# Kernel optimization log

Hardware: AMD Instinct MI355X
Metric: run time of the kernel (lower is better)

Reference implementation:

```python
import jax, jax.numpy as jnp
import numpy as np

N, S, E, H = 8, 1024, 1024, 16
DK = E // H


def setup_inputs() -> dict:
    key = jax.random.key(0)
    ks = jax.random.split(key, 12)
    scale = 1.0 / np.sqrt(E)
    inp = {
        "q": jax.random.normal(ks[0], (N, S, E), jnp.float32),
        "k": jax.random.normal(ks[1], (N, S, E), jnp.float32),
        "v": jax.random.normal(ks[2], (N, S, E), jnp.float32),
        "attn_mask": jax.random.randint(ks[3], (N, S, S), 0, 2).astype(bool),
        "wq": jax.random.normal(ks[4], (E, E), jnp.float32) * scale,
        "bq": jnp.zeros((E,), jnp.float32),
        "wk": jax.random.normal(ks[5], (E, E), jnp.float32) * scale,
        "bk": jnp.zeros((E,), jnp.float32),
        "wv": jax.random.normal(ks[6], (E, E), jnp.float32) * scale,
        "bv": jnp.zeros((E,), jnp.float32),
        "wo": jax.random.normal(ks[7], (E, E), jnp.float32) * scale,
        "bo": jnp.zeros((E,), jnp.float32),
    }
    return inp


def reference(q, k, v, attn_mask, wq, bq, wk, bk, wv, bv, wo, bo):
    # Linear projections (weights stored as (E_in, E_out)), split into heads.
    qh = (q @ wq + bq).reshape(N, S, H, DK).transpose(0, 2, 1, 3)  # (N,H,S,DK)
    kh = (k @ wk + bk).reshape(N, S, H, DK).transpose(0, 2, 1, 3)
    vh = (v @ wv + bv).reshape(N, S, H, DK).transpose(0, 2, 1, 3)
    logits = jnp.einsum("nhsd,nhtd->nhst", qh, kh) / np.sqrt(DK)  # (N,H,S,S)
    eps = 1e9
    logits = jnp.where(attn_mask[:, None, :, :], -eps, logits)
    attn_weights = jax.nn.softmax(logits, axis=-1)
    # dropout layers are identity in eval mode
    o = jnp.einsum("nhst,nhtd->nhsd", attn_weights, vh)  # (N,H,S,DK)
    o = o.transpose(0, 2, 1, 3).reshape(N, S, E)
    o = o @ wo + bo
    return o, attn_weights
```

## Files before the change

kernel.cpp:

```cpp
#include <hip/hip_runtime.h>
#include <cstdint>
#include <cstddef>

#define NB 8
#define SL 1024
#define ED 1024
#define NH 16
#define DKH 64

typedef __attribute__((ext_vector_type(4))) float f32x4;
typedef __attribute__((ext_vector_type(8))) short short8;

__device__ __forceinline__ unsigned short bf16_rn(float x) {
    unsigned int u = __float_as_uint(x);
    u += 0x7FFFu + ((u >> 16) & 1u);
    return (unsigned short)(u >> 16);
}
__device__ __forceinline__ float bf16_f(unsigned short h) {
    return __uint_as_float(((unsigned int)h) << 16);
}
__device__ __forceinline__ void split2(float x, unsigned short& hi, unsigned short& lo) {
    unsigned short h = bf16_rn(x);
    hi = h;
    lo = bf16_rn(x - bf16_f(h));
}

__device__ __forceinline__ void dma16(const unsigned short* src, unsigned short* dst) {
    __builtin_amdgcn_global_load_lds(
        (const __attribute__((address_space(1))) void*)src,
        (__attribute__((address_space(3))) void*)dst,
        16, 0, 0);
}

template<int ROWS>
__device__ __forceinline__ void dma_plane(
    const unsigned short* __restrict__ g, unsigned short* l,
    int ld, int r0, int k0, int wave, int lane)
{
    for (int i = wave; i < ROWS / 16; i += 4) {
        const unsigned short* src =
            g + (size_t)(r0 + i * 16 + (lane >> 2)) * ld + k0 + (lane & 3) * 8;
        dma16(src, l + i * 512);
    }
}

template<bool APRE, int BM, int BN, int WR, int WC, int ROWG, int COLT>
__device__ __forceinline__ void gemm_core3(
    unsigned short* smem,
    const float* __restrict__ Af,
    const unsigned short* __restrict__ Ahg, const unsigned short* __restrict__ Alg,
    int lda,
    const unsigned short* __restrict__ Bhg, const unsigned short* __restrict__ Blg,
    int ldb, int Kd, int m0, int n0,
    f32x4 (&acc)[ROWG][COLT])
{
    static_assert(WR * WC == 4, "4 waves");
    static_assert(16 * ROWG * WR == BM, "rows");
    static_assert(16 * COLT * WC == BN, "cols");
    static_assert(APRE || BM == 128, "fp32 staging assumes BM=128");

    constexpr int ASZ = BM * 32;
    constexpr int BSZ = BN * 32;
    unsigned short* Ah = smem;
    unsigned short* Al = smem + 2 * ASZ;
    unsigned short* Bh = smem + 4 * ASZ;
    unsigned short* Bl = smem + 4 * ASZ + 2 * BSZ;

    const int tid  = threadIdx.x;
    const int wave = tid >> 6;
    const int lane = tid & 63;
    const int quad = lane >> 4;
    const int l16  = lane & 15;
    const int wr   = wave / WC;
    const int wc   = wave % WC;

#pragma unroll
    for (int g = 0; g < ROWG; g++)
#pragma unroll
        for (int jt = 0; jt < COLT; jt++) acc[g][jt] = (f32x4)(0.0f);

    const int ar  = tid >> 1;
    const int acb = (tid & 1) * 2;

    auto load_a = [&](int kk, float4 st[4]) {
        const float* p = Af + (size_t)(m0 + ar) * lda + kk + (tid & 1) * 16;
        st[0] = *(const float4*)(p + 0);
        st[1] = *(const float4*)(p + 4);
        st[2] = *(const float4*)(p + 8);
        st[3] = *(const float4*)(p + 12);
    };
    auto write_a = [&](int b, const float4 st[4]) {
        unsigned short* dh = Ah + b * ASZ;
        unsigned short* dl = Al + b * ASZ;
#pragma unroll
        for (int w = 0; w < 2; w++) {
            const int csw = (acb + w) ^ ((ar >> 1) & 3);
            const float4 u0 = st[2 * w], u1 = st[2 * w + 1];
            short8 h8, l8;
            unsigned short h, l;
            split2(u0.x, h, l); h8[0] = (short)h; l8[0] = (short)l;
            split2(u0.y, h, l); h8[1] = (short)h; l8[1] = (short)l;
            split2(u0.z, h, l); h8[2] = (short)h; l8[2] = (short)l;
            split2(u0.w, h, l); h8[3] = (short)h; l8[3] = (short)l;
            split2(u1.x, h, l); h8[4] = (short)h; l8[4] = (short)l;
            split2(u1.y, h, l); h8[5] = (short)h; l8[5] = (short)l;
            split2(u1.z, h, l); h8[6] = (short)h; l8[6] = (short)l;
            split2(u1.w, h, l); h8[7] = (short)h; l8[7] = (short)l;
            *(short8*)&dh[ar * 32 + csw * 8] = h8;
            *(short8*)&dl[ar * 32 + csw * 8] = l8;
        }
    };
    auto stage_b = [&](int b, int kk) {
        dma_plane<BN>(Bhg, Bh + b * BSZ, ldb, n0, kk, wave, lane);
        dma_plane<BN>(Blg, Bl + b * BSZ, ldb, n0, kk, wave, lane);
    };
    auto stage_a_dma = [&](int b, int kk) {
        dma_plane<BM>(Ahg, Ah + b * ASZ, lda, m0, kk, wave, lane);
        dma_plane<BM>(Alg, Al + b * ASZ, lda, m0, kk, wave, lane);
    };

    if constexpr (APRE) {
        stage_a_dma(0, 0);
    } else {
        float4 st[4];
        load_a(0, st);
        write_a(0, st);
    }
    stage_b(0, 0);
    __syncthreads();

    int buf = 0;
    for (int k0 = 0; k0 < Kd; k0 += 32) {
        const int nk = k0 + 32;
        float4 st[4];
        if (nk < Kd) {
            if constexpr (APRE) stage_a_dma(buf ^ 1, nk);
            else                load_a(nk, st);
            stage_b(buf ^ 1, nk);
        }
        const unsigned short* pAh = Ah + buf * ASZ;
        const unsigned short* pAl = Al + buf * ASZ;
        const unsigned short* pBh = Bh + buf * BSZ;
        const unsigned short* pBl = Bl + buf * BSZ;
        short8 ah[ROWG], al[ROWG];
#pragma unroll
        for (int g = 0; g < ROWG; g++) {
            const int row = wr * (16 * ROWG) + g * 16 + l16;
            int co;
            if constexpr (APRE) co = quad * 8;
            else                co = (quad ^ ((row >> 1) & 3)) * 8;
            ah[g] = *(const short8*)&pAh[row * 32 + co];
            al[g] = *(const short8*)&pAl[row * 32 + co];
        }
#pragma unroll
        for (int jt = 0; jt < COLT; jt++) {
            const int brow = wc * (16 * COLT) + jt * 16 + l16;
            const short8 bh = *(const short8*)&pBh[brow * 32 + quad * 8];
            const short8 bl = *(const short8*)&pBl[brow * 32 + quad * 8];
#pragma unroll
            for (int g = 0; g < ROWG; g++) {
                acc[g][jt] = __builtin_amdgcn_mfma_f32_16x16x32_bf16(al[g], bh, acc[g][jt], 0, 0, 0);
                acc[g][jt] = __builtin_amdgcn_mfma_f32_16x16x32_bf16(ah[g], bl, acc[g][jt], 0, 0, 0);
                acc[g][jt] = __builtin_amdgcn_mfma_f32_16x16x32_bf16(ah[g], bh, acc[g][jt], 0, 0, 0);
            }
        }
        if constexpr (!APRE) {
            if (nk < Kd) write_a(buf ^ 1, st);
        }
        __syncthreads();
        buf ^= 1;
    }
}

__global__ __launch_bounds__(256)
void k_wsplitT(const float* __restrict__ W,
               unsigned short* __restrict__ Th, unsigned short* __restrict__ Tl)
{
    __shared__ float tile[64 * 65];
    const int n0 = blockIdx.x * 64;
    const int k0 = blockIdx.y * 64;
    const int tid = threadIdx.x;
    for (int i = tid; i < 64 * 64; i += 256) {
        const int rk = i >> 6, cn = i & 63;
        tile[rk * 65 + cn] = W[(size_t)(k0 + rk) * ED + n0 + cn];
    }
    __syncthreads();
    for (int i = tid; i < 64 * 64; i += 256) {
        const int rn = i >> 6, ck = i & 63;
        unsigned short h, l;
        split2(tile[ck * 65 + rn], h, l);
        Th[(size_t)(n0 + rn) * ED + k0 + ck] = h;
        Tl[(size_t)(n0 + rn) * ED + k0 + ck] = l;
    }
}

__global__ __launch_bounds__(256)
void k_projQK(const float* __restrict__ X,
              const unsigned short* __restrict__ Wh, const unsigned short* __restrict__ Wl,
              const float* __restrict__ bias,
              unsigned short* __restrict__ Oh, unsigned short* __restrict__ Ol)
{
    __shared__ unsigned short smem[(128 + 128) * 128];
    const int m0 = blockIdx.x * 128;
    const int n0 = blockIdx.y * 128;
    f32x4 acc[4][4];
    gemm_core3<false, 128, 128, 2, 2, 4, 4>(smem, X, nullptr, nullptr, ED,
                                            Wh, Wl, ED, ED, m0, n0, acc);

    const int tid = threadIdx.x, wave = tid >> 6, lane = tid & 63;
    const int quad = lane >> 4, l16 = lane & 15;
    const int wr = wave >> 1, wc = wave & 1;
#pragma unroll
    for (int jt = 0; jt < 4; jt++) {
        const int col = n0 + wc * 64 + jt * 16 + l16;
        const int h = col >> 6, d = col & 63;
        const float b = bias[col];
#pragma unroll
        for (int g = 0; g < 4; g++) {
#pragma unroll
            for (int rr = 0; rr < 4; rr++) {
                const int m = m0 + wr * 64 + g * 16 + quad * 4 + rr;
                const int n = m >> 10, s = m & 1023;
                const size_t idx = (((size_t)(n * NH + h)) * SL + s) * DKH + d;
                unsigned short hh, ll;
                split2(acc[g][jt][rr] + b, hh, ll);
                Oh[idx] = hh;
                Ol[idx] = ll;
            }
        }
    }
}

__global__ __launch_bounds__(256)
void k_projV(const float* __restrict__ X,
             const unsigned short* __restrict__ Wh, const unsigned short* __restrict__ Wl,
             const float* __restrict__ bias,
             unsigned short* __restrict__ Th, unsigned short* __restrict__ Tl)
{
    __shared__ unsigned short smem[(128 + 64) * 128];
    const int m0 = blockIdx.x * 128;
    const int n0 = blockIdx.y * 64;
    f32x4 acc[2][4];
    gemm_core3<false, 128, 64, 4, 1, 2, 4>(smem, X, nullptr, nullptr, ED,
                                           Wh, Wl, ED, ED, m0, n0, acc);

    unsigned int* T = (unsigned int*)smem;
    const int tid = threadIdx.x, wave = tid >> 6, lane = tid & 63;
    const int quad = lane >> 4, l16 = lane & 15;
#pragma unroll
    for (int jt = 0; jt < 4; jt++) {
        const int d = jt * 16 + l16;
        const float b = bias[n0 + d];
#pragma unroll
        for (int g = 0; g < 2; g++) {
#pragma unroll
            for (int rr = 0; rr < 4; rr++) {
                const int sl = wave * 32 + g * 16 + quad * 4 + rr;
                unsigned short hh, ll;
                split2(acc[g][jt][rr] + b, hh, ll);
                T[sl * 65 + d] = (unsigned int)hh | ((unsigned int)ll << 16);
            }
        }
    }
    __syncthreads();
    const int d  = tid >> 2;
    const int sc = (tid & 3) * 32;
    const int ghead = (m0 >> 10) * NH + (n0 >> 6);
    const size_t rowbase = ((size_t)ghead * DKH + d) * SL + (m0 & 1023) + sc;
#pragma unroll
    for (int c = 0; c < 4; c++) {
        short8 h8, l8;
#pragma unroll
        for (int i = 0; i < 8; i++) {
            const unsigned int u = T[(sc + c * 8 + i) * 65 + d];
            h8[i] = (short)(u & 0xFFFFu);
            l8[i] = (short)(u >> 16);
        }
        *(short8*)(Th + rowbase + c * 8) = h8;
        *(short8*)(Tl + rowbase + c * 8) = l8;
    }
}

__global__ __launch_bounds__(256)
void k_logits(const unsigned short* __restrict__ qh_h, const unsigned short* __restrict__ qh_l,
              const unsigned short* __restrict__ kh_h, const unsigned short* __restrict__ kh_l,
              const int* __restrict__ mask, float* __restrict__ attn)
{
    __shared__ unsigned short smem[(128 + 128) * 128];
    const int head = blockIdx.z;
    const int n = head >> 4;
    const int m0 = blockIdx.x * 128;
    const int n0 = blockIdx.y * 128;
    const size_t hb = (size_t)head * SL * DKH;
    f32x4 acc[4][4];
    gemm_core3<true, 128, 128, 2, 2, 4, 4>(smem, nullptr, qh_h + hb, qh_l + hb, DKH,
                                           kh_h + hb, kh_l + hb, DKH, DKH, m0, n0, acc);

    const int tid = threadIdx.x, wave = tid >> 6, lane = tid & 63;
    const int quad = lane >> 4, l16 = lane & 15;
    const int wr = wave >> 1, wc = wave & 1;
    const float scale = 0.125f;
#pragma unroll
    for (int jt = 0; jt < 4; jt++) {
        const int t = n0 + wc * 64 + jt * 16 + l16;
#pragma unroll
        for (int g = 0; g < 4; g++) {
#pragma unroll
            for (int rr = 0; rr < 4; rr++) {
                const int s = m0 + wr * 64 + g * 16 + quad * 4 + rr;
                float vv = acc[g][jt][rr] * scale;
                if (mask[((size_t)n * SL + s) * SL + t]) vv = -1e9f;
                attn[((size_t)head * SL + s) * SL + t] = vv;
            }
        }
    }
}

__global__ __launch_bounds__(256)
void k_softmax(float* __restrict__ attn)
{
    const int tid = threadIdx.x;
    const int wave = tid >> 6, lane = tid & 63;
    const size_t row = (size_t)blockIdx.x * 4 + wave;
    float* p = attn + row * SL;

    float4 v[4];
    float mx = -3.4e38f;
#pragma unroll
    for (int i = 0; i < 4; i++) {
        v[i] = *(const float4*)(p + lane * 4 + i * 256);
        mx = fmaxf(mx, fmaxf(fmaxf(v[i].x, v[i].y), fmaxf(v[i].z, v[i].w)));
    }
#pragma unroll
    for (int o = 32; o > 0; o >>= 1) mx = fmaxf(mx, __shfl_xor(mx, o));

    float sum = 0.0f;
#pragma unroll
    for (int i = 0; i < 4; i++) {
        v[i].x = __expf(v[i].x - mx);
        v[i].y = __expf(v[i].y - mx);
        v[i].z = __expf(v[i].z - mx);
        v[i].w = __expf(v[i].w - mx);
        sum += v[i].x + v[i].y + v[i].z + v[i].w;
    }
#pragma unroll
    for (int o = 32; o > 0; o >>= 1) sum += __shfl_xor(sum, o);

    const float inv = 1.0f / sum;
#pragma unroll
    for (int i = 0; i < 4; i++) {
        v[i].x *= inv; v[i].y *= inv; v[i].z *= inv; v[i].w *= inv;
        *(float4*)(p + lane * 4 + i * 256) = v[i];
    }
}

__global__ __launch_bounds__(256)
void k_pv(const float* __restrict__ attn,
          const unsigned short* __restrict__ vTh, const unsigned short* __restrict__ vTl,
          unsigned short* __restrict__ Oh, unsigned short* __restrict__ Ol)
{
    __shared__ unsigned short smem[(128 + 64) * 128];
    const int head = blockIdx.z;
    const int m0 = blockIdx.x * 128;
    const float* P = attn + (size_t)head * SL * SL;
    const unsigned short* Bh = vTh + (size_t)head * DKH * SL;
    const unsigned short* Bl = vTl + (size_t)head * DKH * SL;
    f32x4 acc[2][4];
    gemm_core3<false, 128, 64, 4, 1, 2, 4>(smem, P, nullptr, nullptr, SL,
                                           Bh, Bl, SL, SL, m0, 0, acc);

    const int tid = threadIdx.x, wave = tid >> 6, lane = tid & 63;
    const int quad = lane >> 4, l16 = lane & 15;
    const int n = head >> 4, h = head & 15;
#pragma unroll
    for (int jt = 0; jt < 4; jt++) {
        const int d = jt * 16 + l16;
#pragma unroll
        for (int g = 0; g < 2; g++) {
#pragma unroll
            for (int rr = 0; rr < 4; rr++) {
                const int s = m0 + wave * 32 + g * 16 + quad * 4 + rr;
                const size_t idx = ((size_t)n * SL + s) * ED + h * DKH + d;
                unsigned short hh, ll;
                split2(acc[g][jt][rr], hh, ll);
                Oh[idx] = hh;
                Ol[idx] = ll;
            }
        }
    }
}

__global__ __launch_bounds__(256)
void k_outproj(const unsigned short* __restrict__ Ah, const unsigned short* __restrict__ Al,
               const unsigned short* __restrict__ Wh, const unsigned short* __restrict__ Wl,
               const float* __restrict__ bias, float* __restrict__ out)
{
    __shared__ unsigned short smem[(128 + 128) * 128];
    const int m0 = blockIdx.x * 128;
    const int n0 = blockIdx.y * 128;
    f32x4 acc[4][4];
    gemm_core3<true, 128, 128, 2, 2, 4, 4>(smem, nullptr, Ah, Al, ED,
                                           Wh, Wl, ED, ED, m0, n0, acc);

    const int tid = threadIdx.x, wave = tid >> 6, lane = tid & 63;
    const int quad = lane >> 4, l16 = lane & 15;
    const int wr = wave >> 1, wc = wave & 1;
#pragma unroll
    for (int jt = 0; jt < 4; jt++) {
        const int col = n0 + wc * 64 + jt * 16 + l16;
        const float b = bias[col];
#pragma unroll
        for (int g = 0; g < 4; g++) {
#pragma unroll
            for (int rr = 0; rr < 4; rr++) {
                const int m = m0 + wr * 64 + g * 16 + quad * 4 + rr;
                out[(size_t)m * ED + col] = acc[g][jt][rr] + b;
            }
        }
    }
}

extern "C" void kernel_launch(void* const* d_in, const int* in_sizes, int n_in,
                              void* d_out, int out_size, void* d_ws, size_t ws_size,
                              hipStream_t stream) {
    const float* q    = (const float*)d_in[0];
    const float* k    = (const float*)d_in[1];
    const float* v    = (const float*)d_in[2];
    const int*   mask = (const int*)d_in[3];
    const float* wq = (const float*)d_in[4];
    const float* bq = (const float*)d_in[5];
    const float* wk = (const float*)d_in[6];
    const float* bk = (const float*)d_in[7];
    const float* wv = (const float*)d_in[8];
    const float* bv = (const float*)d_in[9];
    const float* wo = (const float*)d_in[10];
    const float* bo = (const float*)d_in[11];

    float* out  = (float*)d_out;
    float* attn = out + (size_t)NB * SL * ED;

    unsigned short* w = (unsigned short*)d_ws;
    const size_t WPL = (size_t)ED * ED;
    unsigned short* wqT_h = w + 0 * WPL;
    unsigned short* wqT_l = w + 1 * WPL;
    unsigned short* wkT_h = w + 2 * WPL;
    unsigned short* wkT_l = w + 3 * WPL;
    unsigned short* wvT_h = w + 4 * WPL;
    unsigned short* wvT_l = w + 5 * WPL;
    unsigned short* woT_h = w + 6 * WPL;
    unsigned short* woT_l = w + 7 * WPL;
    unsigned short* base  = w + 8 * WPL;
    const size_t HPL = (size_t)NB * NH * SL * DKH;
    unsigned short* qh_h = base + 0 * HPL;
    unsigned short* qh_l = base + 1 * HPL;
    unsigned short* kh_h = base + 2 * HPL;
    unsigned short* kh_l = base + 3 * HPL;
    unsigned short* vT_h = base + 4 * HPL;
    unsigned short* vT_l = base + 5 * HPL;
    unsigned short* oh_h = qh_h;
    unsigned short* oh_l = qh_l;

    const dim3 blk(256);
    const dim3 gw(ED / 64, ED / 64);
    hipLaunchKernelGGL(k_wsplitT, gw, blk, 0, stream, wq, wqT_h, wqT_l);
    hipLaunchKernelGGL(k_wsplitT, gw, blk, 0, stream, wk, wkT_h, wkT_l);
    hipLaunchKernelGGL(k_wsplitT, gw, blk, 0, stream, wv, wvT_h, wvT_l);
    hipLaunchKernelGGL(k_wsplitT, gw, blk, 0, stream, wo, woT_h, woT_l);

    const dim3 gproj(8192 / 128, ED / 128);
    hipLaunchKernelGGL(k_projQK, gproj, blk, 0, stream, q, wqT_h, wqT_l, bq, qh_h, qh_l);
    hipLaunchKernelGGL(k_projQK, gproj, blk, 0, stream, k, wkT_h, wkT_l, bk, kh_h, kh_l);

    const dim3 gprojV(8192 / 128, ED / 64);
    hipLaunchKernelGGL(k_projV, gprojV, blk, 0, stream, v, wvT_h, wvT_l, bv, vT_h, vT_l);

    const dim3 glog(SL / 128, SL / 128, NB * NH);
    hipLaunchKernelGGL(k_logits, glog, blk, 0, stream, qh_h, qh_l, kh_h, kh_l, mask, attn);

    hipLaunchKernelGGL(k_softmax, dim3(NB * NH * SL / 4), blk, 0, stream, attn);

    const dim3 gpv(SL / 128, 1, NB * NH);
    hipLaunchKernelGGL(k_pv, gpv, blk, 0, stream, attn, vT_h, vT_l, oh_h, oh_l);

    hipLaunchKernelGGL(k_outproj, gproj, blk, 0, stream, oh_h, oh_l, woT_h, woT_l, bo, out);
}
```

Before: 1.495 ms.

## Fuse logits, masked softmax and PV into one attention kernel

Replaces the separate logits, softmax and PV kernels with one fused kernel. Each 512-thread block handles 32 query rows of one head across the full key length, computes masked logits in registers, does a cross-wave softmax reduction through shared memory, writes the attention weights once, and accumulates P@V from the same registers. This removes the write-read-write-read round trips of the 512MB attention matrix through HBM. The cost is that K and V are read straight from global memory with no LDS staging, each block re-reads them, and register pressure is high.

```diff
diff --git a/kernel.cpp b/kernel.cpp
--- a/kernel.cpp
+++ b/kernel.cpp
@@ -10,6 +10,7 @@
 
 typedef __attribute__((ext_vector_type(4))) float f32x4;
 typedef __attribute__((ext_vector_type(8))) short short8;
+typedef __attribute__((ext_vector_type(4))) short short4v;
 
 __device__ __forceinline__ unsigned short bf16_rn(float x) {
     unsigned int u = __float_as_uint(x);
@@ -281,112 +282,209 @@
     }
 }
 
-__global__ __launch_bounds__(256)
-void k_logits(const unsigned short* __restrict__ qh_h, const unsigned short* __restrict__ qh_l,
-              const unsigned short* __restrict__ kh_h, const unsigned short* __restrict__ kh_l,
-              const int* __restrict__ mask, float* __restrict__ attn)
-{
-    __shared__ unsigned short smem[(128 + 128) * 128];
-    const int head = blockIdx.z;
-    const int n = head >> 4;
-    const int m0 = blockIdx.x * 128;
-    const int n0 = blockIdx.y * 128;
-    const size_t hb = (size_t)head * SL * DKH;
-    f32x4 acc[4][4];
-    gemm_core3<true, 128, 128, 2, 2, 4, 4>(smem, nullptr, qh_h + hb, qh_l + hb, DKH,
-                                           kh_h + hb, kh_l + hb, DKH, DKH, m0, n0, acc);
-
+#define PFW 68
+__global__ __launch_bounds__(512)
+void k_attn_fused(const unsigned short* __restrict__ qh_h, const unsigned short* __restrict__ qh_l,
+                  const unsigned short* __restrict__ kh_h, const unsigned short* __restrict__ kh_l,
+                  const unsigned short* __restrict__ vT_h, const unsigned short* __restrict__ vT_l,
+                  const int* __restrict__ mask, float* __restrict__ attn,
+                  unsigned short* __restrict__ Oh, unsigned short* __restrict__ Ol)
+{
+    __shared__ float Pf[8][16][PFW];
+    __shared__ float MX[4][32];
+    __shared__ float SMm[4][32];
+
+    const int head = blockIdx.y;
+    const int n = head >> 4, h = head & 15;
+    const int m0 = blockIdx.x * 32;
     const int tid = threadIdx.x, wave = tid >> 6, lane = tid & 63;
     const int quad = lane >> 4, l16 = lane & 15;
-    const int wr = wave >> 1, wc = wave & 1;
-    const float scale = 0.125f;
-#pragma unroll
-    for (int jt = 0; jt < 4; jt++) {
-        const int t = n0 + wc * 64 + jt * 16 + l16;
-#pragma unroll
-        for (int g = 0; g < 4; g++) {
-#pragma unroll
-            for (int rr = 0; rr < 4; rr++) {
-                const int s = m0 + wr * 64 + g * 16 + quad * 4 + rr;
-                float vv = acc[g][jt][rr] * scale;
-                if (mask[((size_t)n * SL + s) * SL + t]) vv = -1e9f;
-                attn[((size_t)head * SL + s) * SL + t] = vv;
+    const int rg = wave >> 2, cq = wave & 3;
+
+    const size_t hb = (size_t)head * SL * DKH;
+
+    short8 qa_h[2], qa_l[2];
+    {
+        const unsigned short* qrh = qh_h + hb + (size_t)(m0 + rg * 16 + l16) * DKH + quad * 8;
+        const unsigned short* qrl = qh_l + hb + (size_t)(m0 + rg * 16 + l16) * DKH + quad * 8;
+#pragma unroll
+        for (int kc = 0; kc < 2; kc++) {
+            qa_h[kc] = *(const short8*)(qrh + kc * 32);
+            qa_l[kc] = *(const short8*)(qrl + kc * 32);
+        }
+    }
+
+    f32x4 acc[16];
+    {
+        const unsigned short* kbh = kh_h + hb + (size_t)(cq * 256 + l16) * DKH + quad * 8;
+        const unsigned short* kbl = kh_l + hb + (size_t)(cq * 256 + l16) * DKH + quad * 8;
+#pragma unroll
+        for (int tt = 0; tt < 16; tt++) {
+            const size_t toff = (size_t)tt * 16 * DKH;
+            const short8 bh0 = *(const short8*)(kbh + toff);
+            const short8 bl0 = *(const short8*)(kbl + toff);
+            const short8 bh1 = *(const short8*)(kbh + toff + 32);
+            const short8 bl1 = *(const short8*)(kbl + toff + 32);
+            f32x4 a = (f32x4)(0.0f);
+            a = __builtin_amdgcn_mfma_f32_16x16x32_bf16(qa_l[0], bh0, a, 0, 0, 0);
+            a = __builtin_amdgcn_mfma_f32_16x16x32_bf16(qa_h[0], bl0, a, 0, 0, 0);
+            a = __builtin_amdgcn_mfma_f32_16x16x32_bf16(qa_h[0], bh0, a, 0, 0, 0);
+            a = __builtin_amdgcn_mfma_f32_16x16x32_bf16(qa_l[1], bh1, a, 0, 0, 0);
+            a = __builtin_amdgcn_mfma_f32_16x16x32_bf16(qa_h[1], bl1, a, 0, 0, 0);
+            a = __builtin_amdgcn_mfma_f32_16x16x32_bf16(qa_h[1], bh1, a, 0, 0, 0);
+            acc[tt] = a;
+        }
+    }
+
+    const int* mrow0 = mask + ((size_t)n * SL + (m0 + rg * 16 + quad * 4 + 0)) * SL + cq * 256 + l16;
+    const int* mrow1 = mrow0 + SL;
+    const int* mrow2 = mrow1 + SL;
+    const int* mrow3 = mrow2 + SL;
+#pragma unroll
+    for (int tt = 0; tt < 16; tt++) {
+        const int t = tt * 16;
+        float v0 = acc[tt][0] * 0.125f; if (mrow0[t]) v0 = -1e9f; acc[tt][0] = v0;
+        float v1 = acc[tt][1] * 0.125f; if (mrow1[t]) v1 = -1e9f; acc[tt][1] = v1;
+        float v2 = acc[tt][2] * 0.125f; if (mrow2[t]) v2 = -1e9f; acc[tt][2] = v2;
+        float v3 = acc[tt][3] * 0.125f; if (mrow3[t]) v3 = -1e9f; acc[tt][3] = v3;
+    }
+
+    float m4[4];
+#pragma unroll
+    for (int rr = 0; rr < 4; rr++) {
+        float mx = -3.4e38f;
+#pragma unroll
+        for (int tt = 0; tt < 16; tt++) mx = fmaxf(mx, acc[tt][rr]);
+#pragma unroll
+        for (int o = 8; o > 0; o >>= 1) mx = fmaxf(mx, __shfl_xor(mx, o));
+        m4[rr] = mx;
+    }
+    if (l16 < 4) {
+        const float v = (l16 == 0) ? m4[0] : (l16 == 1) ? m4[1] : (l16 == 2) ? m4[2] : m4[3];
+        MX[cq][rg * 16 + quad * 4 + l16] = v;
+    }
+    __syncthreads();
+    float mc[4], sum4[4];
+#pragma unroll
+    for (int rr = 0; rr < 4; rr++) {
+        const int r = rg * 16 + quad * 4 + rr;
+        mc[rr] = fmaxf(fmaxf(MX[0][r], MX[1][r]), fmaxf(MX[2][r], MX[3][r]));
+        sum4[rr] = 0.0f;
+    }
+
+#pragma unroll
+    for (int tt = 0; tt < 16; tt++) {
+#pragma unroll
+        for (int rr = 0; rr < 4; rr++) {
+            const float p = __expf(acc[tt][rr] - mc[rr]);
+            acc[tt][rr] = p;
+            sum4[rr] += p;
+        }
+    }
+#pragma unroll
+    for (int rr = 0; rr < 4; rr++) {
+#pragma unroll
+        for (int o = 8; o > 0; o >>= 1) sum4[rr] += __shfl_xor(sum4[rr], o);
+    }
+    if (l16 < 4) {
+        const float v = (l16 == 0) ? sum4[0] : (l16 == 1) ? sum4[1] : (l16 == 2) ? sum4[2] : sum4[3];
+        SMm[cq][rg * 16 + quad * 4 + l16] = v;
+    }
+    __syncthreads();
+    float inv[4];
+#pragma unroll
+    for (int rr = 0; rr < 4; rr++) {
+        const int r = rg * 16 + quad * 4 + rr;
+        inv[rr] = 1.0f / (SMm[0][r] + SMm[1][r] + SMm[2][r] + SMm[3][r]);
+    }
+
+    f32x4 oac[4];
+#pragma unroll
+    for (int nt = 0; nt < 4; nt++) oac[nt] = (f32x4)(0.0f);
+
+    const unsigned short* vbh = vT_h + (size_t)head * DKH * SL + (size_t)l16 * SL + cq * 256 + quad * 8;
+    const unsigned short* vbl = vT_l + (size_t)head * DKH * SL + (size_t)l16 * SL + cq * 256 + quad * 8;
+    float* aw = attn + ((size_t)head * SL + (m0 + rg * 16)) * SL + cq * 256;
+    const int srow = lane >> 2;
+    const int sseg = (lane & 3) * 16;
+
+#pragma unroll
+    for (int c = 0; c < 4; c++) {
+#pragma unroll
+        for (int i = 0; i < 4; i++) {
+            const int tt = c * 4 + i;
+            Pf[wave][quad * 4 + 0][i * 16 + l16] = acc[tt][0] * inv[0];
+            Pf[wave][quad * 4 + 1][i * 16 + l16] = acc[tt][1] * inv[1];
+            Pf[wave][quad * 4 + 2][i * 16 + l16] = acc[tt][2] * inv[2];
+            Pf[wave][quad * 4 + 3][i * 16 + l16] = acc[tt][3] * inv[3];
+        }
+        {
+            float* dst = aw + (size_t)srow * SL + c * 64 + sseg;
+            const float* srcb = &Pf[wave][srow][sseg];
+            const f32x4 w0 = *(const f32x4*)(srcb + 0);
+            const f32x4 w1 = *(const f32x4*)(srcb + 4);
+            const f32x4 w2 = *(const f32x4*)(srcb + 8);
+            const f32x4 w3 = *(const f32x4*)(srcb + 12);
+            *(f32x4*)(dst + 0)  = w0;
+            *(f32x4*)(dst + 4)  = w1;
+            *(f32x4*)(dst + 8)  = w2;
+            *(f32x4*)(dst + 12) = w3;
+        }
+#pragma unroll
+        for (int ks = 0; ks < 2; ks++) {
+            const float* pr = &Pf[wave][l16][ks * 32 + quad * 8];
+            const f32x4 p0 = *(const f32x4*)(pr + 0);
+            const f32x4 p1 = *(const f32x4*)(pr + 4);
+            short8 ph, pl;
+            {
+                unsigned short hh, ll;
+                split2(p0[0], hh, ll); ph[0] = (short)hh; pl[0] = (short)ll;
+                split2(p0[1], hh, ll); ph[1] = (short)hh; pl[1] = (short)ll;
+                split2(p0[2], hh, ll); ph[2] = (short)hh; pl[2] = (short)ll;
+                split2(p0[3], hh, ll); ph[3] = (short)hh; pl[3] = (short)ll;
+                split2(p1[0], hh, ll); ph[4] = (short)hh; pl[4] = (short)ll;
+                split2(p1[1], hh, ll); ph[5] = (short)hh; pl[5] = (short)ll;
+                split2(p1[2], hh, ll); ph[6] = (short)hh; pl[6] = (short)ll;
+                split2(p1[3], hh, ll); ph[7] = (short)hh; pl[7] = (short)ll;
             }
-        }
-    }
-}
-
-__global__ __launch_bounds__(256)
-void k_softmax(float* __restrict__ attn)
-{
-    const int tid = threadIdx.x;
-    const int wave = tid >> 6, lane = tid & 63;
-    const size_t row = (size_t)blockIdx.x * 4 + wave;
-    float* p = attn + row * SL;
-
-    float4 v[4];
-    float mx = -3.4e38f;
-#pragma unroll
-    for (int i = 0; i < 4; i++) {
-        v[i] = *(const float4*)(p + lane * 4 + i * 256);
-        mx = fmaxf(mx, fmaxf(fmaxf(v[i].x, v[i].y), fmaxf(v[i].z, v[i].w)));
-    }
-#pragma unroll
-    for (int o = 32; o > 0; o >>= 1) mx = fmaxf(mx, __shfl_xor(mx, o));
-
-    float sum = 0.0f;
-#pragma unroll
-    for (int i = 0; i < 4; i++) {
-        v[i].x = __expf(v[i].x - mx);
-        v[i].y = __expf(v[i].y - mx);
-        v[i].z = __expf(v[i].z - mx);
-        v[i].w = __expf(v[i].w - mx);
-        sum += v[i].x + v[i].y + v[i].z + v[i].w;
-    }
-#pragma unroll
-    for (int o = 32; o > 0; o >>= 1) sum += __shfl_xor(sum, o);
-
-    const float inv = 1.0f / sum;
-#pragma unroll
-    for (int i = 0; i < 4; i++) {
-        v[i].x *= inv; v[i].y *= inv; v[i].z *= inv; v[i].w *= inv;
-        *(float4*)(p + lane * 4 + i * 256) = v[i];
-    }
-}
-
-__global__ __launch_bounds__(256)
-void k_pv(const float* __restrict__ attn,
-          const unsigned short* __restrict__ vTh, const unsigned short* __restrict__ vTl,
-          unsigned short* __restrict__ Oh, unsigned short* __restrict__ Ol)
-{
-    __shared__ unsigned short smem[(128 + 64) * 128];
-    const int head = blockIdx.z;
-    const int m0 = blockIdx.x * 128;
-    const float* P = attn + (size_t)head * SL * SL;
-    const unsigned short* Bh = vTh + (size_t)head * DKH * SL;
-    const unsigned short* Bl = vTl + (size_t)head * DKH * SL;
-    f32x4 acc[2][4];
-    gemm_core3<false, 128, 64, 4, 1, 2, 4>(smem, P, nullptr, nullptr, SL,
-                                           Bh, Bl, SL, SL, m0, 0, acc);
-
-    const int tid = threadIdx.x, wave = tid >> 6, lane = tid & 63;
-    const int quad = lane >> 4, l16 = lane & 15;
-    const int n = head >> 4, h = head & 15;
-#pragma unroll
-    for (int jt = 0; jt < 4; jt++) {
-        const int d = jt * 16 + l16;
-#pragma unroll
-        for (int g = 0; g < 2; g++) {
-#pragma unroll
-            for (int rr = 0; rr < 4; rr++) {
-                const int s = m0 + wave * 32 + g * 16 + quad * 4 + rr;
-                const size_t idx = ((size_t)n * SL + s) * ED + h * DKH + d;
-                unsigned short hh, ll;
-                split2(acc[g][jt][rr], hh, ll);
-                Oh[idx] = hh;
-                Ol[idx] = ll;
+            const size_t koff = (size_t)(c * 64 + ks * 32);
+#pragma unroll
+            for (int nt = 0; nt < 4; nt++) {
+                const short8 bh = *(const short8*)(vbh + (size_t)nt * 16 * SL + koff);
+                const short8 bl = *(const short8*)(vbl + (size_t)nt * 16 * SL + koff);
+                oac[nt] = __builtin_amdgcn_mfma_f32_16x16x32_bf16(pl, bh, oac[nt], 0, 0, 0);
+                oac[nt] = __builtin_amdgcn_mfma_f32_16x16x32_bf16(ph, bl, oac[nt], 0, 0, 0);
+                oac[nt] = __builtin_amdgcn_mfma_f32_16x16x32_bf16(ph, bh, oac[nt], 0, 0, 0);
             }
         }
+    }
+
+    __syncthreads();
+#pragma unroll
+    for (int nt = 0; nt < 4; nt++) {
+        Pf[wave][quad * 4 + 0][nt * 16 + l16] = oac[nt][0];
+        Pf[wave][quad * 4 + 1][nt * 16 + l16] = oac[nt][1];
+        Pf[wave][quad * 4 + 2][nt * 16 + l16] = oac[nt][2];
+        Pf[wave][quad * 4 + 3][nt * 16 + l16] = oac[nt][3];
+    }
+    __syncthreads();
+    {
+        const int r  = tid >> 4;
+        const int dc = (tid & 15) * 4;
+        const int rgc = r >> 4, rl = r & 15;
+        short4v h4, l4;
+#pragma unroll
+        for (int i = 0; i < 4; i++) {
+            const float v = Pf[rgc * 4 + 0][rl][dc + i] + Pf[rgc * 4 + 1][rl][dc + i]
+                          + Pf[rgc * 4 + 2][rl][dc + i] + Pf[rgc * 4 + 3][rl][dc + i];
+            unsigned short hh, ll;
+            split2(v, hh, ll);
+            h4[i] = (short)hh;
+            l4[i] = (short)ll;
+        }
+        const size_t oidx = ((size_t)n * SL + (m0 + r)) * ED + h * DKH + dc;
+        *(short4v*)(Oh + oidx) = h4;
+        *(short4v*)(Ol + oidx) = l4;
     }
 }
 
@@ -474,13 +572,9 @@
     const dim3 gprojV(8192 / 128, ED / 64);
     hipLaunchKernelGGL(k_projV, gprojV, blk, 0, stream, v, wvT_h, wvT_l, bv, vT_h, vT_l);
 
-    const dim3 glog(SL / 128, SL / 128, NB * NH);
-    hipLaunchKernelGGL(k_logits, glog, blk, 0, stream, qh_h, qh_l, kh_h, kh_l, mask, attn);
-
-    hipLaunchKernelGGL(k_softmax, dim3(NB * NH * SL / 4), blk, 0, stream, attn);
-
-    const dim3 gpv(SL / 128, 1, NB * NH);
-    hipLaunchKernelGGL(k_pv, gpv, blk, 0, stream, attn, vT_h, vT_l, oh_h, oh_l);
+    const dim3 gfa(SL / 32, NB * NH);
+    hipLaunchKernelGGL(k_attn_fused, gfa, dim3(512), 0, stream,
+                       qh_h, qh_l, kh_h, kh_l, vT_h, vT_l, mask, attn, oh_h, oh_l);
 
     hipLaunchKernelGGL(k_outproj, gproj, blk, 0, stream, oh_h, oh_l, woT_h, woT_l, bo, out);
 }
```

After: 1.561 ms. 4.5% more time.
